# Optimization experiments

Hardware: AMD Instinct MI355X
Metric: run time of the kernel (lower is better)

## Reference

```python
import jax, jax.numpy as jnp
import numpy as np

N_E = 1024
E_DIM = 64
BETA = 0.25
DECAY = 0.99
EPSILON = 1e-5


def setup_inputs() -> dict:
    key = jax.random.key(0)
    k1, k2, k3 = jax.random.split(key, 3)
    z = jax.random.normal(k1, (32, E_DIM, 32, 32), dtype=jnp.float32)
    # codebook initialized uniform(-1/n_e, 1/n_e) as in the torch module
    emb_w = jax.random.uniform(k2, (N_E, E_DIM), minval=-1.0 / N_E, maxval=1.0 / N_E, dtype=jnp.float32)
    ema_cluster_size = jnp.ones((N_E,), dtype=jnp.float32)
    ema_w = jax.random.uniform(k3, (N_E, E_DIM), minval=-1.0 / N_E, maxval=1.0 / N_E, dtype=jnp.float32)
    return {"z": z, "emb_w": emb_w, "ema_cluster_size": ema_cluster_size, "ema_w": ema_w}


def reference(z, emb_w, ema_cluster_size, ema_w):
    B, C, H, W = z.shape  # C == E_DIM
    zf = jnp.transpose(z, (0, 2, 3, 1)).reshape(-1, E_DIM)  # [N, e_dim]
    N = zf.shape[0]

    # squared-distance via ||z||^2 + ||e||^2 - 2 z.e (same expansion as torch code)
    d = (jnp.sum(zf * zf, axis=1, keepdims=True)
         + jnp.sum(emb_w * emb_w, axis=1)
         - 2.0 * zf @ emb_w.T)  # [N, n_e]
    idx = jnp.argmin(d, axis=1)  # [N]

    min_encodings = jax.nn.one_hot(idx, N_E, dtype=jnp.float32)  # [N, n_e]
    # cluster stats via scatter-add (equivalent to one-hot matmuls, cheaper)
    cluster_size = jax.ops.segment_sum(jnp.ones((N,), jnp.float32), idx, num_segments=N_E)
    sum_encodings = jax.ops.segment_sum(zf, idx, num_segments=N_E)  # [n_e, e_dim]

    # EMA update (training path, done before the z_q lookup as in torch)
    new_cs = DECAY * ema_cluster_size + (1.0 - DECAY) * cluster_size
    new_w = DECAY * ema_w + (1.0 - DECAY) * sum_encodings
    n = jnp.sum(new_cs)
    cs_norm = (new_cs + EPSILON) / (n + N_E * EPSILON) * n
    new_emb = new_w / cs_norm[:, None]  # updated codebook

    z_q = new_emb[idx].reshape(B, H, W, C).transpose(0, 3, 1, 2)  # [B,C,H,W]
    loss = BETA * jnp.mean((jax.lax.stop_gradient(z_q) - z) ** 2)
    z_q_st = z + jax.lax.stop_gradient(z_q - z)  # straight-through

    avg_probs = cluster_size / N
    perplexity = jnp.exp(-jnp.sum(avg_probs * jnp.log(avg_probs + 1e-10)))
    return loss, z_q_st, perplexity, min_encodings, idx
```

## Files before the change

### kernel.cpp

```cpp
#include <hip/hip_runtime.h>
#include <math.h>

#define NVEC 32768
#define NE   1024
#define ED   64
#define TOT  2097152
#define NCHUNK 8
#define CHUNK  128
#define MT     64

#define O_LOSS   0
#define O_ZQ     1
#define O_PERP   2097153
#define O_MINENC 2097154
#define O_IDX    35651586

#define W_PIDX   0
#define W_CS     32768
#define W_SUMENC 33792
#define W_NEWEMB 99328
#define W_LOSSP  164864

__global__ void __launch_bounds__(256, 3) k_dist(const float* __restrict__ z,
                                                 const float* __restrict__ emb,
                                                 int* __restrict__ fidx,
                                                 float* __restrict__ out) {
    __shared__ __align__(16) float s_a[64 * 64];
    __shared__ __align__(16) float s_b[64 * 132];
    __shared__ float s_esq[CHUNK];
    __shared__ float s_zsq[MT];

    int tid = threadIdx.x;
    int n0 = blockIdx.x * MT;
    int b = n0 >> 10, hw0 = n0 & 1023;
    const float* zb = z + b * 65536 + hw0;

#pragma unroll
    for (int j = 0; j < 4; ++j) {
        int f4i = j * 256 + tid;
        int c = f4i >> 4, pos = (f4i & 15) * 4;
        float4 v = *(const float4*)(zb + (c << 10) + pos);
        v.x = __fmul_rn(2.0f, v.x);
        v.y = __fmul_rn(2.0f, v.y);
        v.z = __fmul_rn(2.0f, v.z);
        v.w = __fmul_rn(2.0f, v.w);
        *(float4*)(s_a + c * 64 + pos) = v;
    }
    __syncthreads();

    if (tid < MT) {
        float r[8];
#pragma unroll
        for (int j = 0; j < 8; ++j) {
            float v = s_a[j * 64 + tid];
            r[j] = __fmul_rn(v, v);
        }
#pragma unroll
        for (int i = 8; i < 64; i += 8)
#pragma unroll
            for (int j = 0; j < 8; ++j) {
                float v = s_a[(i + j) * 64 + tid];
                r[j] = __fadd_rn(r[j], __fmul_rn(v, v));
            }
        s_zsq[tid] = __fmul_rn(0.25f, __fadd_rn(
            __fadd_rn(__fadd_rn(r[0], r[1]), __fadd_rn(r[2], r[3])),
            __fadd_rn(__fadd_rn(r[4], r[5]), __fadd_rn(r[6], r[7]))));
    }
    __syncthreads();

    int mi = tid & 15, ki = tid >> 4;
    int mbase = mi * 4, kbase = ki * 8;
    float zs[4];
#pragma unroll
    for (int mu = 0; mu < 4; ++mu) zs[mu] = s_zsq[mbase + mu];

    float bd[4];
    int bix[4];
#pragma unroll
    for (int mu = 0; mu < 4; ++mu) { bd[mu] = 3.4e38f; bix[mu] = kbase; }

    for (int q = 0; q < NCHUNK; ++q) {
        int k0 = q * CHUNK;
        __syncthreads();
#pragma unroll
        for (int j = 0; j < 8; ++j) {
            int f4i = j * 256 + tid;
            int kl = f4i >> 4, c4 = f4i & 15;
            float4 v = *(const float4*)(emb + (size_t)(k0 + kl) * ED + c4 * 4);
            int base = ((( kl >> 2) + c4) & 31) * 4 + (kl & 3);
            s_b[(c4 * 4 + 0) * 132 + base] = v.x;
            s_b[(c4 * 4 + 1) * 132 + base] = v.y;
            s_b[(c4 * 4 + 2) * 132 + base] = v.z;
            s_b[(c4 * 4 + 3) * 132 + base] = v.w;
        }
        if (tid < CHUNK) {
            const float* ep = emb + (size_t)(k0 + tid) * ED;
            float r[8];
#pragma unroll
            for (int j = 0; j < 8; ++j) r[j] = __fmul_rn(ep[j], ep[j]);
#pragma unroll
            for (int i = 8; i < 64; i += 8)
#pragma unroll
                for (int j = 0; j < 8; ++j)
                    r[j] = __fadd_rn(r[j], __fmul_rn(ep[i + j], ep[i + j]));
            s_esq[tid] = __fadd_rn(
                __fadd_rn(__fadd_rn(r[0], r[1]), __fadd_rn(r[2], r[3])),
                __fadd_rn(__fadd_rn(r[4], r[5]), __fadd_rn(r[6], r[7])));
        }
        __syncthreads();

        float acc[4][8];
#pragma unroll
        for (int mu = 0; mu < 4; ++mu)
#pragma unroll
            for (int ku = 0; ku < 8; ++ku) acc[mu][ku] = 0.f;

#pragma unroll 4
        for (int c = 0; c < 64; ++c) {
            int c4 = c >> 2;
            float4 av = *(const float4*)(s_a + c * 64 + mbase);
            float4 b0 = *(const float4*)(s_b + c * 132 + ((2 * ki + c4) & 31) * 4);
            float4 b1 = *(const float4*)(s_b + c * 132 + ((2 * ki + 1 + c4) & 31) * 4);
#pragma unroll
            for (int mu = 0; mu < 4; ++mu) {
                float a = (&av.x)[mu];
                acc[mu][0] = __fmaf_rn(a, b0.x, acc[mu][0]);
                acc[mu][1] = __fmaf_rn(a, b0.y, acc[mu][1]);
                acc[mu][2] = __fmaf_rn(a, b0.z, acc[mu][2]);
                acc[mu][3] = __fmaf_rn(a, b0.w, acc[mu][3]);
                acc[mu][4] = __fmaf_rn(a, b1.x, acc[mu][4]);
                acc[mu][5] = __fmaf_rn(a, b1.y, acc[mu][5]);
                acc[mu][6] = __fmaf_rn(a, b1.z, acc[mu][6]);
                acc[mu][7] = __fmaf_rn(a, b1.w, acc[mu][7]);
            }
        }

#pragma unroll
        for (int mu = 0; mu < 4; ++mu)
#pragma unroll
            for (int ku = 0; ku < 8; ++ku) {
                float d = __fsub_rn(__fadd_rn(zs[mu], s_esq[kbase + ku]),
                                    acc[mu][ku]);
                if (d < bd[mu]) { bd[mu] = d; bix[mu] = k0 + kbase + ku; }
            }
    }

    __syncthreads();
    float* red_d = s_b;
    int* red_i = (int*)(s_b + 1024);
#pragma unroll
    for (int mu = 0; mu < 4; ++mu) {
        red_d[ki * 64 + mbase + mu] = bd[mu];
        red_i[ki * 64 + mbase + mu] = bix[mu];
    }
    __syncthreads();
    if (tid < MT) {
        float best = red_d[tid];
        int bi = red_i[tid];
#pragma unroll
        for (int q = 1; q < 16; ++q) {
            float d = red_d[q * 64 + tid];
            int i = red_i[q * 64 + tid];
            if (d < best || (d == best && i < bi)) { best = d; bi = i; }
        }
        fidx[n0 + tid] = bi;
        out[O_IDX + n0 + tid] = (float)bi;
    }
}

__global__ void __launch_bounds__(256) k_sumenc(const int* __restrict__ idx,
                                                const float* __restrict__ z,
                                                float* __restrict__ cs,
                                                float* __restrict__ sumenc) {
    int k = blockIdx.x;
    int wave = threadIdx.x >> 6, lane = threadIdx.x & 63;
    float acc = 0.f;
    int cnt = 0;
    int base = wave * 8192;
    for (int it = 0; it < 128; ++it) {
        int n0 = base + it * 64;
        int idv = idx[n0 + lane];
        unsigned long long m = __ballot(idv == k);
        cnt += __popcll(m);
        while (m) {
            int bit = __ffsll((unsigned long long)m) - 1;
            m &= m - 1;
            int n = n0 + bit;
            int b = n >> 10, hw = n & 1023;
            acc = __fadd_rn(acc, z[b * 65536 + lane * 1024 + hw]);
        }
    }
    __shared__ float sacc[4][64];
    __shared__ int scnt[4];
    sacc[wave][lane] = acc;
    if (lane == 0) scnt[wave] = cnt;
    __syncthreads();
    if (wave == 0) {
        float t = __fadd_rn(__fadd_rn(sacc[0][lane], sacc[1][lane]),
                            __fadd_rn(sacc[2][lane], sacc[3][lane]));
        sumenc[k * ED + lane] = t;
        if (lane == 0) cs[k] = (float)(scnt[0] + scnt[1] + scnt[2] + scnt[3]);
    }
}

__global__ void __launch_bounds__(1024) k_ema(const float* __restrict__ ema_cs,
                                              const float* __restrict__ ema_w,
                                              const float* __restrict__ cs,
                                              const float* __restrict__ sumenc,
                                              float* __restrict__ newemb,
                                              float* __restrict__ out) {
    int k = threadIdx.x;
    float c = cs[k];
    float ncs = 0.99f * ema_cs[k] + (1.0f - 0.99f) * c;
    float p = c * (1.0f / (float)NVEC);
    float e = p * logf(p + 1e-10f);
    float rn_ = ncs, re_ = e;
#pragma unroll
    for (int o = 32; o > 0; o >>= 1) {
        rn_ += __shfl_down(rn_, o, 64);
        re_ += __shfl_down(re_, o, 64);
    }
    __shared__ float sn[16], se_[16];
    __shared__ float s_n;
    int wave = k >> 6, lane = k & 63;
    if (lane == 0) { sn[wave] = rn_; se_[wave] = re_; }
    __syncthreads();
    if (k == 0) {
        float tn = 0.f, te = 0.f;
#pragma unroll
        for (int w = 0; w < 16; ++w) { tn += sn[w]; te += se_[w]; }
        s_n = tn;
        out[O_PERP] = expf(-te);
    }
    __syncthreads();
    float nt = s_n;
    float csn = (ncs + 1e-5f) / (nt + 1024.0f * 1e-5f) * nt;
    __shared__ float s_csn[NE];
    s_csn[k] = csn;
    __syncthreads();
    for (int t = k; t < NE * ED; t += 1024) {
        float nw = 0.99f * ema_w[t] + (1.0f - 0.99f) * sumenc[t];
        newemb[t] = nw / s_csn[t >> 6];
    }
}

__global__ void __launch_bounds__(256) k_zq(const float* __restrict__ z,
                                            const int* __restrict__ idx,
                                            const float* __restrict__ newemb,
                                            float* __restrict__ out,
                                            float* __restrict__ lossp) {
    __shared__ int sbi[16];
    if (threadIdx.x < 16) sbi[threadIdx.x] = idx[blockIdx.x * 16 + threadIdx.x];
    __syncthreads();

    float local = 0.f;
#pragma unroll
    for (int i = 0; i < 4; ++i) {
        int t = blockIdx.x * 256 + threadIdx.x + i * 524288;
        int b = t >> 16, c = (t >> 10) & 63, hw = t & 1023;
        int n = (b << 10) | hw;
        float e = newemb[idx[n] * ED + c];
        float zv = z[t];
        float diff = e - zv;
        out[O_ZQ + t] = zv + diff;
        local = fmaf(diff, diff, local);
    }

    int t = threadIdx.x;
    int r0 = blockIdx.x * 16;
    for (int r = 0; r < 16; ++r) {
        int rbi = sbi[r];
        float* rp = out + O_MINENC + (size_t)(r0 + r) * NE;
        if (t < 254) {
            int col = 2 + t * 4;
            float4 v;
            v.x = (col == rbi) ? 1.0f : 0.0f;
            v.y = (col + 1 == rbi) ? 1.0f : 0.0f;
            v.z = (col + 2 == rbi) ? 1.0f : 0.0f;
            v.w = (col + 3 == rbi) ? 1.0f : 0.0f;
            *(float4*)(rp + col) = v;
        } else if (t == 254) {
            float2 v;
            v.x = (0 == rbi) ? 1.0f : 0.0f;
            v.y = (1 == rbi) ? 1.0f : 0.0f;
            *(float2*)(rp) = v;
        } else {
            float4 v;
            v.x = (1018 == rbi) ? 1.0f : 0.0f;
            v.y = (1019 == rbi) ? 1.0f : 0.0f;
            v.z = (1020 == rbi) ? 1.0f : 0.0f;
            v.w = (1021 == rbi) ? 1.0f : 0.0f;
            *(float4*)(rp + 1018) = v;
            float2 w;
            w.x = (1022 == rbi) ? 1.0f : 0.0f;
            w.y = (1023 == rbi) ? 1.0f : 0.0f;
            *(float2*)(rp + 1022) = w;
        }
    }

#pragma unroll
    for (int o = 32; o > 0; o >>= 1) local += __shfl_down(local, o, 64);
    __shared__ float sp[4];
    int wave = threadIdx.x >> 6;
    if ((threadIdx.x & 63) == 0) sp[wave] = local;
    __syncthreads();
    if (threadIdx.x == 0)
        lossp[blockIdx.x] = (sp[0] + sp[1]) + (sp[2] + sp[3]);
}

__global__ void __launch_bounds__(256) k_fin(const float* __restrict__ lossp,
                                             float* __restrict__ out) {
    float v = 0.f;
#pragma unroll
    for (int i = 0; i < 8; ++i) v += lossp[i * 256 + threadIdx.x];
#pragma unroll
    for (int o = 32; o > 0; o >>= 1) v += __shfl_down(v, o, 64);
    __shared__ float sp[4];
    int wave = threadIdx.x >> 6;
    if ((threadIdx.x & 63) == 0) sp[wave] = v;
    __syncthreads();
    if (threadIdx.x == 0)
        out[O_LOSS] = 0.25f * (((sp[0] + sp[1]) + (sp[2] + sp[3])) * (1.0f / (float)TOT));
}

extern "C" void kernel_launch(void* const* d_in, const int* in_sizes, int n_in,
                              void* d_out, int out_size, void* d_ws, size_t ws_size,
                              hipStream_t stream) {
    const float* z      = (const float*)d_in[0];
    const float* emb    = (const float*)d_in[1];
    const float* ema_cs = (const float*)d_in[2];
    const float* ema_w  = (const float*)d_in[3];
    float* out = (float*)d_out;
    float* ws  = (float*)d_ws;

    k_dist<<<512, 256, 0, stream>>>(z, emb, (int*)(ws + W_PIDX), out);
    k_sumenc<<<NE, 256, 0, stream>>>((const int*)(ws + W_PIDX), z, ws + W_CS,
                                     ws + W_SUMENC);
    k_ema<<<1, 1024, 0, stream>>>(ema_cs, ema_w, ws + W_CS, ws + W_SUMENC,
                                  ws + W_NEWEMB, out);
    k_zq<<<2048, 256, 0, stream>>>(z, (const int*)(ws + W_PIDX), ws + W_NEWEMB, out,
                                   ws + W_LOSSP);
    k_fin<<<1, 256, 0, stream>>>(ws + W_LOSSP, out);
}
```

Measured before the change: 286.0 us.

## Precompute codebook norms once, prefetch next chunk, fold loss reduction into k_zq

k_dist now computes all 1024 codebook squared norms once up front instead of per chunk. It also prefetches the next codebook chunk into registers while the current chunk is staged in shared memory, so global loads overlap with compute. The final loss reduction moves into the last k_zq block via an atomic ticket, which is reset in k_ema, and the separate k_fin launch is removed. The trade-off is higher register pressure from the prefetch buffers and extra shared memory for the full norm array.

```diff
diff --git a/kernel.cpp b/kernel.cpp
--- a/kernel.cpp
+++ b/kernel.cpp
@@ -20,6 +20,7 @@
 #define W_SUMENC 33792
 #define W_NEWEMB 99328
 #define W_LOSSP  164864
+#define W_TICKET 166912
 
 __global__ void __launch_bounds__(256, 3) k_dist(const float* __restrict__ z,
                                                  const float* __restrict__ emb,
@@ -27,7 +28,7 @@
                                                  float* __restrict__ out) {
     __shared__ __align__(16) float s_a[64 * 64];
     __shared__ __align__(16) float s_b[64 * 132];
-    __shared__ float s_esq[CHUNK];
+    __shared__ float s_esq[NE];
     __shared__ float s_zsq[MT];
 
     int tid = threadIdx.x;
@@ -46,6 +47,22 @@
         v.w = __fmul_rn(2.0f, v.w);
         *(float4*)(s_a + c * 64 + pos) = v;
     }
+#pragma unroll
+    for (int j = 0; j < 4; ++j) {
+        int k = j * 256 + tid;
+        const float* ep = emb + (size_t)k * ED;
+        float r[8];
+#pragma unroll
+        for (int u = 0; u < 8; ++u) r[u] = __fmul_rn(ep[u], ep[u]);
+#pragma unroll
+        for (int i = 8; i < 64; i += 8)
+#pragma unroll
+            for (int u = 0; u < 8; ++u)
+                r[u] = __fadd_rn(r[u], __fmul_rn(ep[i + u], ep[i + u]));
+        s_esq[k] = __fadd_rn(
+            __fadd_rn(__fadd_rn(r[0], r[1]), __fadd_rn(r[2], r[3])),
+            __fadd_rn(__fadd_rn(r[4], r[5]), __fadd_rn(r[6], r[7])));
+    }
     __syncthreads();
 
     if (tid < MT) {
@@ -79,36 +96,39 @@
 #pragma unroll
     for (int mu = 0; mu < 4; ++mu) { bd[mu] = 3.4e38f; bix[mu] = kbase; }
 
+    int s_kl[8], s_c4[8];
+#pragma unroll
+    for (int j = 0; j < 8; ++j) {
+        int f4i = j * 256 + tid;
+        s_kl[j] = f4i >> 4;
+        s_c4[j] = f4i & 15;
+    }
+
+    float4 pf[8];
+#pragma unroll
+    for (int j = 0; j < 8; ++j)
+        pf[j] = *(const float4*)(emb + (size_t)s_kl[j] * ED + s_c4[j] * 4);
+
     for (int q = 0; q < NCHUNK; ++q) {
+        __syncthreads();
+#pragma unroll
+        for (int j = 0; j < 8; ++j) {
+            int kl = s_kl[j], c4 = s_c4[j];
+            int base = (((kl >> 2) + c4) & 31) * 4 + (kl & 3);
+            s_b[(c4 * 4 + 0) * 132 + base] = pf[j].x;
+            s_b[(c4 * 4 + 1) * 132 + base] = pf[j].y;
+            s_b[(c4 * 4 + 2) * 132 + base] = pf[j].z;
+            s_b[(c4 * 4 + 3) * 132 + base] = pf[j].w;
+        }
+        if (q + 1 < NCHUNK) {
+            const float* nb = emb + (size_t)(q + 1) * CHUNK * ED;
+#pragma unroll
+            for (int j = 0; j < 8; ++j)
+                pf[j] = *(const float4*)(nb + (size_t)s_kl[j] * ED + s_c4[j] * 4);
+        }
+        __syncthreads();
+
         int k0 = q * CHUNK;
-        __syncthreads();
-#pragma unroll
-        for (int j = 0; j < 8; ++j) {
-            int f4i = j * 256 + tid;
-            int kl = f4i >> 4, c4 = f4i & 15;
-            float4 v = *(const float4*)(emb + (size_t)(k0 + kl) * ED + c4 * 4);
-            int base = ((( kl >> 2) + c4) & 31) * 4 + (kl & 3);
-            s_b[(c4 * 4 + 0) * 132 + base] = v.x;
-            s_b[(c4 * 4 + 1) * 132 + base] = v.y;
-            s_b[(c4 * 4 + 2) * 132 + base] = v.z;
-            s_b[(c4 * 4 + 3) * 132 + base] = v.w;
-        }
-        if (tid < CHUNK) {
-            const float* ep = emb + (size_t)(k0 + tid) * ED;
-            float r[8];
-#pragma unroll
-            for (int j = 0; j < 8; ++j) r[j] = __fmul_rn(ep[j], ep[j]);
-#pragma unroll
-            for (int i = 8; i < 64; i += 8)
-#pragma unroll
-                for (int j = 0; j < 8; ++j)
-                    r[j] = __fadd_rn(r[j], __fmul_rn(ep[i + j], ep[i + j]));
-            s_esq[tid] = __fadd_rn(
-                __fadd_rn(__fadd_rn(r[0], r[1]), __fadd_rn(r[2], r[3])),
-                __fadd_rn(__fadd_rn(r[4], r[5]), __fadd_rn(r[6], r[7])));
-        }
-        __syncthreads();
-
         float acc[4][8];
 #pragma unroll
         for (int mu = 0; mu < 4; ++mu)
@@ -139,7 +159,7 @@
         for (int mu = 0; mu < 4; ++mu)
 #pragma unroll
             for (int ku = 0; ku < 8; ++ku) {
-                float d = __fsub_rn(__fadd_rn(zs[mu], s_esq[kbase + ku]),
+                float d = __fsub_rn(__fadd_rn(zs[mu], s_esq[k0 + kbase + ku]),
                                     acc[mu][ku]);
                 if (d < bd[mu]) { bd[mu] = d; bix[mu] = k0 + kbase + ku; }
             }
@@ -208,8 +228,10 @@
                                               const float* __restrict__ cs,
                                               const float* __restrict__ sumenc,
                                               float* __restrict__ newemb,
+                                              int* __restrict__ ticket,
                                               float* __restrict__ out) {
     int k = threadIdx.x;
+    if (k == 0) *ticket = 0;
     float c = cs[k];
     float ncs = 0.99f * ema_cs[k] + (1.0f - 0.99f) * c;
     float p = c * (1.0f / (float)NVEC);
@@ -248,7 +270,8 @@
                                             const int* __restrict__ idx,
                                             const float* __restrict__ newemb,
                                             float* __restrict__ out,
-                                            float* __restrict__ lossp) {
+                                            float* __restrict__ lossp,
+                                            int* __restrict__ ticket) {
     __shared__ int sbi[16];
     if (threadIdx.x < 16) sbi[threadIdx.x] = idx[blockIdx.x * 16 + threadIdx.x];
     __syncthreads();
@@ -304,23 +327,27 @@
     int wave = threadIdx.x >> 6;
     if ((threadIdx.x & 63) == 0) sp[wave] = local;
     __syncthreads();
-    if (threadIdx.x == 0)
+    __shared__ int s_last;
+    if (threadIdx.x == 0) {
         lossp[blockIdx.x] = (sp[0] + sp[1]) + (sp[2] + sp[3]);
-}
-
-__global__ void __launch_bounds__(256) k_fin(const float* __restrict__ lossp,
-                                             float* __restrict__ out) {
-    float v = 0.f;
-#pragma unroll
-    for (int i = 0; i < 8; ++i) v += lossp[i * 256 + threadIdx.x];
-#pragma unroll
-    for (int o = 32; o > 0; o >>= 1) v += __shfl_down(v, o, 64);
-    __shared__ float sp[4];
-    int wave = threadIdx.x >> 6;
-    if ((threadIdx.x & 63) == 0) sp[wave] = v;
-    __syncthreads();
-    if (threadIdx.x == 0)
-        out[O_LOSS] = 0.25f * (((sp[0] + sp[1]) + (sp[2] + sp[3])) * (1.0f / (float)TOT));
+        __threadfence();
+        s_last = (atomicAdd(ticket, 1) == 2047);
+    }
+    __syncthreads();
+    if (s_last) {
+        __threadfence();
+        float v = 0.f;
+#pragma unroll
+        for (int i = 0; i < 8; ++i) v += lossp[i * 256 + threadIdx.x];
+#pragma unroll
+        for (int o = 32; o > 0; o >>= 1) v += __shfl_down(v, o, 64);
+        __shared__ float sq[4];
+        if ((threadIdx.x & 63) == 0) sq[wave] = v;
+        __syncthreads();
+        if (threadIdx.x == 0)
+            out[O_LOSS] = 0.25f * (((sq[0] + sq[1]) + (sq[2] + sq[3])) *
+                                   (1.0f / (float)TOT));
+    }
 }
 
 extern "C" void kernel_launch(void* const* d_in, const int* in_sizes, int n_in,
@@ -337,8 +364,7 @@
     k_sumenc<<<NE, 256, 0, stream>>>((const int*)(ws + W_PIDX), z, ws + W_CS,
                                      ws + W_SUMENC);
     k_ema<<<1, 1024, 0, stream>>>(ema_cs, ema_w, ws + W_CS, ws + W_SUMENC,
-                                  ws + W_NEWEMB, out);
+                                  ws + W_NEWEMB, (int*)(ws + W_TICKET), out);
     k_zq<<<2048, 256, 0, stream>>>(z, (const int*)(ws + W_PIDX), ws + W_NEWEMB, out,
-                                   ws + W_LOSSP);
-    k_fin<<<1, 256, 0, stream>>>(ws + W_LOSSP, out);
-}
+                                   ws + W_LOSSP, (int*)(ws + W_TICKET));
+}
```

Result: slower. 403.0 us (+40.9%).
